# Optimization experiments

Measured on AMD Instinct MI355X. Metric: run time of the kernel, lower is better.

## Reference

```python
import jax, jax.numpy as jnp
import numpy as np

N_NODES = 100000
N_EDGES = 1600000
D = 128          # gnn_input_size == gnn_hidden_size
N_LAYERS = 7
N_GRAPHS = 64
N_CLASSES = 10
SNN_IN, SNN_H = 512, 1024
SNN_BETA = 0.85


def setup_inputs() -> dict:
    key = jax.random.key(0)
    ks = jax.random.split(key, 16)
    s = 0.05  # keep activations tame through 7 relu layers
    return {
        "snn_x": jax.random.normal(ks[0], (N_GRAPHS, SNN_IN), jnp.float32),
        "x": jax.random.normal(ks[1], (N_NODES, D), jnp.float32),
        "edge_index": jax.random.randint(ks[2], (2, N_EDGES), 0, N_NODES, jnp.int64),
        "batch": jnp.sort(jax.random.randint(ks[3], (N_NODES,), 0, N_GRAPHS, jnp.int64)),
        "snn_w1": jax.random.normal(ks[4], (SNN_IN, SNN_H), jnp.float32) * s,
        "snn_b1": jax.random.normal(ks[5], (SNN_H,), jnp.float32) * s,
        "snn_w2": jax.random.normal(ks[6], (SNN_H, N_CLASSES), jnp.float32) * s,
        "snn_b2": jax.random.normal(ks[7], (N_CLASSES,), jnp.float32) * s,
        "conv_wrel": jax.random.normal(ks[8], (N_LAYERS, D, D), jnp.float32) * s,
        "conv_wroot": jax.random.normal(ks[9], (N_LAYERS, D, D), jnp.float32) * s,
        "conv_brel": jax.random.normal(ks[10], (N_LAYERS, D), jnp.float32) * s,
        "lin_w": jax.random.normal(ks[11], (D, N_CLASSES), jnp.float32) * s,
        "lin_b": jax.random.normal(ks[12], (N_CLASSES,), jnp.float32) * s,
        "fuse_w": jax.random.normal(ks[13], (2 * N_CLASSES, N_CLASSES), jnp.float32) * s,
        "fuse_b": jax.random.normal(ks[14], (N_CLASSES,), jnp.float32) * s,
    }


def reference(snn_x, x, edge_index, batch,
              snn_w1, snn_b1, snn_w2, snn_b2,
              conv_wrel, conv_wroot, conv_brel,
              lin_w, lin_b, fuse_w, fuse_b):
    n = x.shape[0]
    src, dst = edge_index[0], edge_index[1]
    h = x
    for i in range(conv_wrel.shape[0]):
        agg = jax.ops.segment_sum(h[src], dst, num_segments=n)  # gather + scatter-add
        h = jax.nn.relu(agg @ conv_wrel[i] + conv_brel[i] + h @ conv_wroot[i])
    # global_mean_pool over batch segments
    sums = jax.ops.segment_sum(h, batch, num_segments=N_GRAPHS)
    cnts = jax.ops.segment_sum(jnp.ones((n,), h.dtype), batch, num_segments=N_GRAPHS)
    pooled = sums / jnp.maximum(cnts, 1.0)[:, None]
    gnn_logits = pooled @ lin_w + lin_b
    # SNN branch
    snn_h = jax.nn.relu(snn_x @ snn_w1 + snn_b1)
    snn_logits = SNN_BETA * (snn_h @ snn_w2 + snn_b2)
    # fusion
    fused = jnp.concatenate([snn_logits, gnn_logits], axis=-1)
    return fused @ fuse_w + fuse_b
```

## Files before the change

kernel.cpp:

```cpp
#include <hip/hip_runtime.h>
#include <hip/hip_bf16.h>

#define N_NODES 100000
#define N_EDGES 1600000
#define DIM     128
#define N_LAYERS 7
#define N_GRAPHS 64
#define SNN_IN  512
#define SNN_HID 1024
#define NCLS    10
#define M_PAD   100096
#define MBLK    782
#define NBK     782
#define SORT_CHUNK 4096
#define SORT_NCH   391
#define XPAIRS  (N_NODES * 64)
#define WELEMS  (N_LAYERS * DIM * 256)
#define AGG_BLOCKS 2048
#define AGG_WAVES  (AGG_BLOCKS * 4)
#define POOL_NB 782

typedef __attribute__((ext_vector_type(8))) short short8;
typedef __attribute__((ext_vector_type(4))) float f32x4;

__device__ __forceinline__ unsigned int f2bf(float f) {
    unsigned int u = __float_as_uint(f);
    return (u + 0x7fffu + ((u >> 16) & 1u)) >> 16;
}
__device__ __forceinline__ float bf2f(unsigned short b) {
    return __uint_as_float(((unsigned int)b) << 16);
}
__device__ __forceinline__ void acc_pair(unsigned int u, float& lo, float& hi) {
    lo += __uint_as_float(u << 16);
    hi += __uint_as_float(u & 0xffff0000u);
}

__global__ void k_convert(const float* __restrict__ x, const float* __restrict__ wrel,
                          const float* __restrict__ wroot, unsigned int* __restrict__ h,
                          unsigned short* __restrict__ Wt,
                          float* __restrict__ pooled, int* __restrict__ counts) {
    int i = blockIdx.x * blockDim.x + threadIdx.x;
    if (i < N_GRAPHS * 128) pooled[i] = 0.f;
    if (i >= N_GRAPHS * 128 && i < N_GRAPHS * 129) counts[i - N_GRAPHS * 128] = 0;
    if (i < XPAIRS) {
        float2 v = ((const float2*)x)[i];
        h[i] = f2bf(v.x) | (f2bf(v.y) << 16);
    } else {
        int idx = i - XPAIRS;
        if (idx < WELEMS) {
            int l = idx >> 15, rem = idx & 32767, n = rem >> 8, k = rem & 255;
            float v = (k < 128) ? wrel[l * 16384 + k * 128 + n]
                                : wroot[l * 16384 + (k - 128) * 128 + n];
            Wt[idx] = (unsigned short)f2bf(v);
        }
    }
}

__global__ __launch_bounds__(256) void k_histA(const int* __restrict__ dst,
                                               int* __restrict__ chunk_hist) {
    __shared__ int hist[NBK];
    int b = blockIdx.x, t = threadIdx.x;
    int e0 = b * SORT_CHUNK;
    int e1 = e0 + SORT_CHUNK; if (e1 > N_EDGES) e1 = N_EDGES;
    for (int i = t; i < NBK; i += 256) hist[i] = 0;
    __syncthreads();
    for (int e = e0 + t; e < e1; e += 256) atomicAdd(&hist[dst[e] >> 7], 1);
    __syncthreads();
    for (int i = t; i < NBK; i += 256) chunk_hist[b * NBK + i] = hist[i];
}

__global__ __launch_bounds__(64) void k_colscan(int* __restrict__ chunk_hist,
                                                int* __restrict__ btot) {
    int b = blockIdx.x;
    int lane = threadIdx.x;
    const int C = (SORT_NCH + 63) / 64;
    int vals[C]; int sum = 0;
    #pragma unroll
    for (int j = 0; j < C; j++) {
        int c = lane * C + j;
        vals[j] = (c < SORT_NCH) ? chunk_hist[c * NBK + b] : 0;
        sum += vals[j];
    }
    int s = sum;
    #pragma unroll
    for (int o = 1; o < 64; o <<= 1) { int t = __shfl_up(s, o); if (lane >= o) s += t; }
    if (lane == 63) btot[b] = s;
    int run = s - sum;
    #pragma unroll
    for (int j = 0; j < C; j++) {
        int c = lane * C + j;
        if (c < SORT_NCH) chunk_hist[c * NBK + b] = run;
        run += vals[j];
    }
}

__global__ __launch_bounds__(256) void k_bscan(const int* __restrict__ btot,
                                               int* __restrict__ bucket_base) {
    __shared__ int wsum[4];
    int tid = threadIdx.x, lane = tid & 63, wid = tid >> 6;
    int i0 = tid * 4;
    int v[4]; int sum = 0;
    #pragma unroll
    for (int j = 0; j < 4; j++) { int i = i0 + j; v[j] = (i < NBK) ? btot[i] : 0; sum += v[j]; }
    int s = sum;
    #pragma unroll
    for (int o = 1; o < 64; o <<= 1) { int t = __shfl_up(s, o); if (lane >= o) s += t; }
    if (lane == 63) wsum[wid] = s;
    __syncthreads();
    if (tid == 0) {
        int acc = 0;
        #pragma unroll
        for (int w = 0; w < 4; w++) { acc += wsum[w]; wsum[w] = acc; }
    }
    __syncthreads();
    int prefix = s - sum + (wid ? wsum[wid - 1] : 0);
    #pragma unroll
    for (int j = 0; j < 4; j++) { int i = i0 + j; if (i < NBK) bucket_base[i] = prefix; prefix += v[j]; }
}

__global__ __launch_bounds__(256) void k_scatterA(const int* __restrict__ src,
                                                  const int* __restrict__ dst,
                                                  const int* __restrict__ chunk_hist,
                                                  const int* __restrict__ bucket_base,
                                                  unsigned int* __restrict__ pairs) {
    __shared__ int lcur[NBK];
    int b = blockIdx.x, t = threadIdx.x;
    int e0 = b * SORT_CHUNK;
    int e1 = e0 + SORT_CHUNK; if (e1 > N_EDGES) e1 = N_EDGES;
    for (int i = t; i < NBK; i += 256) lcur[i] = chunk_hist[b * NBK + i] + bucket_base[i];
    __syncthreads();
    for (int e = e0 + t; e < e1; e += 256) {
        int d = dst[e];
        int bk = d >> 7;
        int pos = atomicAdd(&lcur[bk], 1);
        pairs[pos] = (unsigned int)src[e] | ((unsigned int)(d & 127) << 17);
    }
}

__global__ __launch_bounds__(256) void k_bucketB(const unsigned int* __restrict__ pairs,
                                                 const int* __restrict__ bucket_base,
                                                 const int* __restrict__ btot,
                                                 int* __restrict__ row_off,
                                                 int* __restrict__ sorted_src) {
    __shared__ int lcnt[128];
    __shared__ int loff[128];
    int b = blockIdx.x, t = threadIdx.x;
    int node0 = b << 7;
    int nn = N_NODES - node0; if (nn > 128) nn = 128;
    int base = bucket_base[b];
    int end  = base + btot[b];
    if (t < 128) lcnt[t] = 0;
    __syncthreads();
    for (int i = base + t; i < end; i += 256) atomicAdd(&lcnt[pairs[i] >> 17], 1);
    __syncthreads();
    if (t < 64) {
        int v0 = lcnt[2 * t], v1 = lcnt[2 * t + 1];
        int s = v0 + v1, ps = s;
        #pragma unroll
        for (int o = 1; o < 64; o <<= 1) { int u = __shfl_up(ps, o); if (t >= o) ps += u; }
        int excl = ps - s;
        loff[2 * t] = excl; loff[2 * t + 1] = excl + v0;
    }
    __syncthreads();
    if (t < nn) row_off[node0 + t] = base + loff[t];
    if (b == NBK - 1 && t == 0) row_off[N_NODES] = end;
    if (t < 128) lcnt[t] = 0;
    __syncthreads();
    for (int i = base + t; i < end; i += 256) {
        unsigned int p = pairs[i];
        int l = p >> 17;
        int pos = atomicAdd(&lcnt[l], 1);
        sorted_src[base + loff[l] + pos] = (int)(p & 0x1FFFFu);
    }
}

__global__ __launch_bounds__(256) void k_agg(const uint4* __restrict__ h4,
                                             const int* __restrict__ row_off,
                                             const int* __restrict__ sorted_src,
                                             uint4* __restrict__ agg4) {
    int gw = blockIdx.x * 4 + (threadIdx.x >> 6);
    int lane = threadIdx.x & 63;
    int sub = lane >> 4, li = lane & 15;
    for (int node = gw; node < N_NODES; node += AGG_WAVES) {
        int beg = row_off[node], end = row_off[node + 1];
        float a[8] = {0.f, 0.f, 0.f, 0.f, 0.f, 0.f, 0.f, 0.f};
        for (int base = beg; base < end; base += 16) {
            int sidx[4]; bool val[4];
            #pragma unroll
            for (int u = 0; u < 4; u++) {
                int e = base + 4 * u + sub;
                val[u] = e < end;
                sidx[u] = val[u] ? sorted_src[e] : 0;
            }
            uint4 r[4];
            #pragma unroll
            for (int u = 0; u < 4; u++) {
                if (val[u]) r[u] = h4[(size_t)sidx[u] * 16 + li];
                else        r[u] = make_uint4(0u, 0u, 0u, 0u);
            }
            #pragma unroll
            for (int u = 0; u < 4; u++) {
                acc_pair(r[u].x, a[0], a[1]); acc_pair(r[u].y, a[2], a[3]);
                acc_pair(r[u].z, a[4], a[5]); acc_pair(r[u].w, a[6], a[7]);
            }
        }
        #pragma unroll
        for (int i = 0; i < 8; i++) {
            a[i] += __shfl_xor(a[i], 16);
            a[i] += __shfl_xor(a[i], 32);
        }
        if (sub == 0) {
            uint4 o;
            o.x = f2bf(a[0]) | (f2bf(a[1]) << 16);
            o.y = f2bf(a[2]) | (f2bf(a[3]) << 16);
            o.z = f2bf(a[4]) | (f2bf(a[5]) << 16);
            o.w = f2bf(a[6]) | (f2bf(a[7]) << 16);
            agg4[(size_t)node * 16 + li] = o;
        }
    }
}

__global__ __launch_bounds__(256) void k_gemm(const unsigned short* __restrict__ Ag,
                                              const unsigned short* __restrict__ H,
                                              const unsigned short* __restrict__ Wt,
                                              const float* __restrict__ bias,
                                              unsigned short* __restrict__ Hout) {
    __shared__ unsigned short Es[64 * 144];
    int tid = threadIdx.x;
    int lane = tid & 63, wid = tid >> 6;
    int wr = (wid >> 1) * 64, wc = (wid & 1) * 64;
    int row0 = blockIdx.x * 128;
    f32x4 acc[4][4] = {};

    int ksub = (lane >> 4) * 8;
    const unsigned short* Aga = Ag + (size_t)(row0 + wr + (lane & 15)) * 128 + ksub;
    const unsigned short* Ha  = H  + (size_t)(row0 + wr + (lane & 15)) * 128 + ksub;
    const unsigned short* Bb  = Wt + (size_t)(wc + (lane & 15)) * 256 + ksub;

    auto load_frags = [&](short8* a, short8* b, int s) {
        const unsigned short* ab = (s < 4 ? Aga : Ha) + (s & 3) * 32;
        #pragma unroll
        for (int mi = 0; mi < 4; mi++) a[mi] = *(const short8*)(ab + mi * 16 * 128);
        const unsigned short* bp = Bb + s * 32;
        #pragma unroll
        for (int ni = 0; ni < 4; ni++) b[ni] = *(const short8*)(bp + ni * 16 * 256);
    };
    auto do_mfma = [&](short8* a, short8* b) {
        #pragma unroll
        for (int mi = 0; mi < 4; mi++)
            #pragma unroll
            for (int ni = 0; ni < 4; ni++)
                acc[mi][ni] = __builtin_amdgcn_mfma_f32_16x16x32_bf16(a[mi], b[ni], acc[mi][ni], 0, 0, 0);
    };

    short8 a0[4], b0[4], a1[4], b1[4];
    load_frags(a0, b0, 0);
    #pragma unroll
    for (int s = 0; s < 8; s += 2) {
        load_frags(a1, b1, s + 1);
        do_mfma(a0, b0);
        if (s + 2 < 8) load_frags(a0, b0, s + 2);
        do_mfma(a1, b1);
    }

    int cb = wc + (lane & 15);
    int rs = (lane >> 4) * 4;
    #pragma unroll
    for (int p = 0; p < 2; ++p) {
        __syncthreads();
        if (wr == 64 * p) {
            #pragma unroll
            for (int ni = 0; ni < 4; ni++) {
                int col = cb + ni * 16;
                float bn = bias[col];
                #pragma unroll
                for (int mi = 0; mi < 4; mi++) {
                    int rloc = mi * 16 + rs;
                    #pragma unroll
                    for (int rr = 0; rr < 4; rr++) {
                        float v = acc[mi][ni][rr] + bn;
                        v = v > 0.f ? v : 0.f;
                        Es[(rloc + rr) * 144 + col] = (unsigned short)f2bf(v);
                    }
                }
            }
        }
        __syncthreads();
        int rloc = tid >> 2;
        int c4 = (tid & 3) * 4;
        uint4* gd = (uint4*)(Hout + (size_t)(row0 + 64 * p + rloc) * 128);
        const uint4* es = (const uint4*)(Es + (size_t)rloc * 144);
        #pragma unroll
        for (int j = 0; j < 4; j++) gd[c4 + j] = es[c4 + j];
    }
}

__global__ __launch_bounds__(256) void k_pool_snn(const unsigned short* __restrict__ h,
                                                  const int* __restrict__ batch,
                                                  float* __restrict__ pooled,
                                                  int* __restrict__ counts,
                                                  const float* __restrict__ x,
                                                  const float* __restrict__ w1,
                                                  const float* __restrict__ b1,
                                                  float* __restrict__ snn_out) {
    if (blockIdx.x < POOL_NB) {
        __shared__ int bsh[128];
        int start = blockIdx.x * 128;
        int t = threadIdx.x & 127;
        int half = threadIdx.x >> 7;
        if (half == 0) {
            int end = start + 128; if (end > N_NODES) end = N_NODES;
            int nn = end - start;
            if (t < nn) bsh[t] = batch[start + t];
        }
        __syncthreads();
        if (half == 1) {
            int end = start + 128; if (end > N_NODES) end = N_NODES;
            int nn = end - start;
            float acc = 0.f; int cur = -1, cnt = 0;
            for (int i = 0; i < nn; i++) {
                int g = bsh[i];
                if (g != cur) {
                    if (cur >= 0) { atomicAdd(&pooled[cur * 128 + t], acc); if (t == 0) atomicAdd(&counts[cur], cnt); }
                    cur = g; acc = 0.f; cnt = 0;
                }
                acc += bf2f(h[(size_t)(start + i) * 128 + t]);
                cnt++;
            }
            if (cur >= 0) { atomicAdd(&pooled[cur * 128 + t], acc); if (t == 0) atomicAdd(&counts[cur], cnt); }
        } else {
            int end = start + 128; if (end > N_NODES) end = N_NODES;
            int nn = end - start;
            float acc = 0.f; int cur = -1;
            int td = t + 0;
            (void)nn; (void)acc; (void)cur; (void)td;
        }
    } else {
        int m = blockIdx.x - POOL_NB;
        __shared__ float xs[SNN_IN];
        int tid = threadIdx.x;
        for (int i = tid; i < SNN_IN; i += 256) xs[i] = x[m * SNN_IN + i];
        __syncthreads();
        float a0 = 0.f, a1 = 0.f, a2 = 0.f, a3 = 0.f;
        for (int k = 0; k < SNN_IN; k++) {
            float xv = xs[k];
            const float* wr = w1 + (size_t)k * SNN_HID + tid;
            a0 += xv * wr[0]; a1 += xv * wr[256]; a2 += xv * wr[512]; a3 += xv * wr[768];
        }
        float v;
        v = a0 + b1[tid];       snn_out[m * SNN_HID + tid]       = v > 0.f ? v : 0.f;
        v = a1 + b1[tid + 256]; snn_out[m * SNN_HID + tid + 256] = v > 0.f ? v : 0.f;
        v = a2 + b1[tid + 512]; snn_out[m * SNN_HID + tid + 512] = v > 0.f ? v : 0.f;
        v = a3 + b1[tid + 768]; snn_out[m * SNN_HID + tid + 768] = v > 0.f ? v : 0.f;
    }
}

__global__ __launch_bounds__(64) void k_head(const float* __restrict__ pooled, const int* __restrict__ counts,
                                             const float* __restrict__ lin_w, const float* __restrict__ lin_b,
                                             const float* __restrict__ snn_h, const float* __restrict__ w2,
                                             const float* __restrict__ b2, const float* __restrict__ fuse_w,
                                             const float* __restrict__ fuse_b, float* __restrict__ out) {
    int m = blockIdx.x, lane = threadIdx.x;
    __shared__ float sm[20];
    float cnt = (float)(counts[m] > 0 ? counts[m] : 1);
    float p0 = pooled[m * 128 + lane] / cnt;
    float p1 = pooled[m * 128 + 64 + lane] / cnt;
    for (int c = 0; c < NCLS; c++) {
        float v = p0 * lin_w[lane * 10 + c] + p1 * lin_w[(lane + 64) * 10 + c];
        #pragma unroll
        for (int o = 32; o > 0; o >>= 1) v += __shfl_down(v, o);
        if (lane == 0) sm[10 + c] = v + lin_b[c];
    }
    for (int c = 0; c < NCLS; c++) {
        float v = 0.f;
        #pragma unroll
        for (int j = 0; j < 16; j++) {
            int k = lane + j * 64;
            v += snn_h[m * SNN_HID + k] * w2[k * 10 + c];
        }
        #pragma unroll
        for (int o = 32; o > 0; o >>= 1) v += __shfl_down(v, o);
        if (lane == 0) sm[c] = 0.85f * (v + b2[c]);
    }
    __syncthreads();
    if (lane < NCLS) {
        float o = fuse_b[lane];
        #pragma unroll
        for (int j = 0; j < 20; j++) o += sm[j] * fuse_w[j * 10 + lane];
        out[m * 10 + lane] = o;
    }
}

extern "C" void kernel_launch(void* const* d_in, const int* in_sizes, int n_in,
                              void* d_out, int out_size, void* d_ws, size_t ws_size,
                              hipStream_t stream) {
    const float* snn_x  = (const float*)d_in[0];
    const float* x      = (const float*)d_in[1];
    const int*   ei     = (const int*)d_in[2];
    const int*   batch  = (const int*)d_in[3];
    const float* w1     = (const float*)d_in[4];
    const float* b1     = (const float*)d_in[5];
    const float* w2     = (const float*)d_in[6];
    const float* b2     = (const float*)d_in[7];
    const float* wrel   = (const float*)d_in[8];
    const float* wroot  = (const float*)d_in[9];
    const float* brel   = (const float*)d_in[10];
    const float* lin_w  = (const float*)d_in[11];
    const float* lin_b  = (const float*)d_in[12];
    const float* fuse_w = (const float*)d_in[13];
    const float* fuse_b = (const float*)d_in[14];
    const int* srcv = ei;
    const int* dstv = ei + N_EDGES;

    char* ws = (char*)d_ws;
    size_t off = 0;
    auto alloc = [&](size_t b) { char* p = ws + off; off = (off + b + 255) & ~(size_t)255; return p; };
    unsigned short* h0   = (unsigned short*)alloc((size_t)M_PAD * 128 * 2);
    unsigned short* h1   = (unsigned short*)alloc((size_t)M_PAD * 128 * 2);
    unsigned short* agg  = (unsigned short*)alloc((size_t)M_PAD * 128 * 2);
    unsigned short* Wt   = (unsigned short*)alloc((size_t)N_LAYERS * 128 * 256 * 2);
    int* sorted_src = (int*)alloc((size_t)N_EDGES * 4);
    unsigned int* pairs = (unsigned int*)alloc((size_t)N_EDGES * 4);
    int* chunk_hist = (int*)alloc((size_t)SORT_NCH * NBK * 4);
    int* row_off    = (int*)alloc((size_t)(N_NODES + 1) * 4);
    int* btot       = (int*)alloc((size_t)NBK * 4);
    int* bucket_base= (int*)alloc((size_t)NBK * 4);
    float* pooled   = (float*)alloc((size_t)N_GRAPHS * 128 * 4);
    int* counts     = (int*)alloc((size_t)N_GRAPHS * 4);
    float* snn_h    = (float*)alloc((size_t)N_GRAPHS * SNN_HID * 4);

    k_histA<<<SORT_NCH, 256, 0, stream>>>(dstv, chunk_hist);
    k_colscan<<<NBK, 64, 0, stream>>>(chunk_hist, btot);
    k_bscan<<<1, 256, 0, stream>>>(btot, bucket_base);
    k_scatterA<<<SORT_NCH, 256, 0, stream>>>(srcv, dstv, chunk_hist, bucket_base, pairs);
    k_bucketB<<<NBK, 256, 0, stream>>>(pairs, bucket_base, btot, row_off, sorted_src);
    k_convert<<<(XPAIRS + WELEMS + 255) / 256, 256, 0, stream>>>(x, wrel, wroot, (unsigned int*)h0,
                                                                 Wt, pooled, counts);

    unsigned short* hc = h0;
    unsigned short* hn = h1;
    for (int l = 0; l < N_LAYERS; l++) {
        k_agg<<<AGG_BLOCKS, 256, 0, stream>>>((const uint4*)hc, row_off, sorted_src, (uint4*)agg);
        k_gemm<<<MBLK, 256, 0, stream>>>(agg, hc, Wt + (size_t)l * 128 * 256, brel + l * 128, hn);
        unsigned short* t = hc; hc = hn; hn = t;
    }
    k_pool_snn<<<POOL_NB + N_GRAPHS, 256, 0, stream>>>(hc, batch, pooled, counts,
                                                       snn_x, w1, b1, snn_h);
    k_head<<<N_GRAPHS, 64, 0, stream>>>(pooled, counts, lin_w, lin_b, snn_h, w2, b2, fuse_w, fuse_b,
                                        (float*)d_out);
}
```

Before: 924.8 us.

## Pad CSR rows to multiples of four and aggregate four nodes per wave

```diff
diff --git a/kernel.cpp b/kernel.cpp
--- a/kernel.cpp
+++ b/kernel.cpp
@@ -15,10 +15,13 @@
 #define SORT_CHUNK 4096
 #define SORT_NCH   391
 #define XPAIRS  (N_NODES * 64)
+#define HPAIRS  (M_PAD * 64)
 #define WELEMS  (N_LAYERS * DIM * 256)
 #define AGG_BLOCKS 2048
 #define AGG_WAVES  (AGG_BLOCKS * 4)
+#define NQUAD   (N_NODES / 4)
 #define POOL_NB 782
+#define SS_PAD  2000384
 
 typedef __attribute__((ext_vector_type(8))) short short8;
 typedef __attribute__((ext_vector_type(4))) float f32x4;
@@ -45,8 +48,10 @@
     if (i < XPAIRS) {
         float2 v = ((const float2*)x)[i];
         h[i] = f2bf(v.x) | (f2bf(v.y) << 16);
+    } else if (i < HPAIRS) {
+        h[i] = 0u;
     } else {
-        int idx = i - XPAIRS;
+        int idx = i - HPAIRS;
         if (idx < WELEMS) {
             int l = idx >> 15, rem = idx & 32767, n = rem >> 8, k = rem & 255;
             float v = (k < 128) ? wrel[l * 16384 + k * 128 + n]
@@ -141,6 +146,7 @@
                                                  const int* __restrict__ bucket_base,
                                                  const int* __restrict__ btot,
                                                  int* __restrict__ row_off,
+                                                 int* __restrict__ ndeg,
                                                  int* __restrict__ sorted_src) {
     __shared__ int lcnt[128];
     __shared__ int loff[128];
@@ -149,12 +155,13 @@
     int nn = N_NODES - node0; if (nn > 128) nn = 128;
     int base = bucket_base[b];
     int end  = base + btot[b];
+    int pbase = ((base + 3) & ~3) + 512 * b;
     if (t < 128) lcnt[t] = 0;
     __syncthreads();
     for (int i = base + t; i < end; i += 256) atomicAdd(&lcnt[pairs[i] >> 17], 1);
     __syncthreads();
     if (t < 64) {
-        int v0 = lcnt[2 * t], v1 = lcnt[2 * t + 1];
+        int v0 = (lcnt[2 * t] + 3) & ~3, v1 = (lcnt[2 * t + 1] + 3) & ~3;
         int s = v0 + v1, ps = s;
         #pragma unroll
         for (int o = 1; o < 64; o <<= 1) { int u = __shfl_up(ps, o); if (t >= o) ps += u; }
@@ -162,61 +169,81 @@
         loff[2 * t] = excl; loff[2 * t + 1] = excl + v0;
     }
     __syncthreads();
-    if (t < nn) row_off[node0 + t] = base + loff[t];
-    if (b == NBK - 1 && t == 0) row_off[N_NODES] = end;
+    if (t < nn) {
+        int d = lcnt[t];
+        row_off[node0 + t] = pbase + loff[t];
+        ndeg[node0 + t] = d;
+        int pad = (d + 3) & ~3;
+        for (int k = d; k < pad; k++) sorted_src[pbase + loff[t] + k] = N_NODES;
+    }
+    __syncthreads();
     if (t < 128) lcnt[t] = 0;
     __syncthreads();
     for (int i = base + t; i < end; i += 256) {
         unsigned int p = pairs[i];
         int l = p >> 17;
         int pos = atomicAdd(&lcnt[l], 1);
-        sorted_src[base + loff[l] + pos] = (int)(p & 0x1FFFFu);
-    }
-}
-
-__global__ __launch_bounds__(256) void k_agg(const uint4* __restrict__ h4,
+        sorted_src[pbase + loff[l] + pos] = (int)(p & 0x1FFFFu);
+    }
+}
+
+#define GATH(d0, d1, d2, d3, s) \
+    d0 = *(const uint4*)(hbl + (size_t)(((unsigned)(s).x) << 8)); \
+    d1 = *(const uint4*)(hbl + (size_t)(((unsigned)(s).y) << 8)); \
+    d2 = *(const uint4*)(hbl + (size_t)(((unsigned)(s).z) << 8)); \
+    d3 = *(const uint4*)(hbl + (size_t)(((unsigned)(s).w) << 8));
+#define ACC4(r0, r1, r2, r3) \
+    acc_pair((r0).x, a[0], a[1]); acc_pair((r0).y, a[2], a[3]); \
+    acc_pair((r0).z, a[4], a[5]); acc_pair((r0).w, a[6], a[7]); \
+    acc_pair((r1).x, a[0], a[1]); acc_pair((r1).y, a[2], a[3]); \
+    acc_pair((r1).z, a[4], a[5]); acc_pair((r1).w, a[6], a[7]); \
+    acc_pair((r2).x, a[0], a[1]); acc_pair((r2).y, a[2], a[3]); \
+    acc_pair((r2).z, a[4], a[5]); acc_pair((r2).w, a[6], a[7]); \
+    acc_pair((r3).x, a[0], a[1]); acc_pair((r3).y, a[2], a[3]); \
+    acc_pair((r3).z, a[4], a[5]); acc_pair((r3).w, a[6], a[7]);
+
+__global__ __launch_bounds__(256) void k_agg(const char* __restrict__ hb,
                                              const int* __restrict__ row_off,
-                                             const int* __restrict__ sorted_src,
+                                             const int* __restrict__ ndeg,
+                                             const int4* __restrict__ sorted4,
                                              uint4* __restrict__ agg4) {
     int gw = blockIdx.x * 4 + (threadIdx.x >> 6);
     int lane = threadIdx.x & 63;
     int sub = lane >> 4, li = lane & 15;
-    for (int node = gw; node < N_NODES; node += AGG_WAVES) {
-        int beg = row_off[node], end = row_off[node + 1];
+    const char* hbl = hb + li * 16;
+    for (int quad = gw; quad < NQUAD; quad += AGG_WAVES) {
+        int node = quad * 4 + sub;
+        int beg = row_off[node] >> 2;
+        int nit = (ndeg[node] + 3) >> 2;
         float a[8] = {0.f, 0.f, 0.f, 0.f, 0.f, 0.f, 0.f, 0.f};
-        for (int base = beg; base < end; base += 16) {
-            int sidx[4]; bool val[4];
-            #pragma unroll
-            for (int u = 0; u < 4; u++) {
-                int e = base + 4 * u + sub;
-                val[u] = e < end;
-                sidx[u] = val[u] ? sorted_src[e] : 0;
+        if (nit > 0) {
+            int4 sa = sorted4[beg];
+            int4 sb = sorted4[beg + 1];
+            uint4 A0, A1, A2, A3, B0, B1, B2, B3;
+            GATH(A0, A1, A2, A3, sa);
+            int it = 0;
+            for (; it + 2 < nit; it += 2) {
+                GATH(B0, B1, B2, B3, sb);
+                sa = sorted4[beg + it + 2];
+                ACC4(A0, A1, A2, A3);
+                GATH(A0, A1, A2, A3, sa);
+                sb = sorted4[beg + it + 3];
+                ACC4(B0, B1, B2, B3);
             }
-            uint4 r[4];
-            #pragma unroll
-            for (int u = 0; u < 4; u++) {
-                if (val[u]) r[u] = h4[(size_t)sidx[u] * 16 + li];
-                else        r[u] = make_uint4(0u, 0u, 0u, 0u);
+            if (it + 1 < nit) {
+                GATH(B0, B1, B2, B3, sb);
+                ACC4(A0, A1, A2, A3);
+                ACC4(B0, B1, B2, B3);
+            } else {
+                ACC4(A0, A1, A2, A3);
             }
-            #pragma unroll
-            for (int u = 0; u < 4; u++) {
-                acc_pair(r[u].x, a[0], a[1]); acc_pair(r[u].y, a[2], a[3]);
-                acc_pair(r[u].z, a[4], a[5]); acc_pair(r[u].w, a[6], a[7]);
-            }
-        }
-        #pragma unroll
-        for (int i = 0; i < 8; i++) {
-            a[i] += __shfl_xor(a[i], 16);
-            a[i] += __shfl_xor(a[i], 32);
-        }
-        if (sub == 0) {
-            uint4 o;
-            o.x = f2bf(a[0]) | (f2bf(a[1]) << 16);
-            o.y = f2bf(a[2]) | (f2bf(a[3]) << 16);
-            o.z = f2bf(a[4]) | (f2bf(a[5]) << 16);
-            o.w = f2bf(a[6]) | (f2bf(a[7]) << 16);
-            agg4[(size_t)node * 16 + li] = o;
-        }
+        }
+        uint4 o;
+        o.x = f2bf(a[0]) | (f2bf(a[1]) << 16);
+        o.y = f2bf(a[2]) | (f2bf(a[3]) << 16);
+        o.z = f2bf(a[4]) | (f2bf(a[5]) << 16);
+        o.w = f2bf(a[6]) | (f2bf(a[7]) << 16);
+        agg4[(size_t)node * 16 + li] = o;
     }
 }
 
@@ -280,6 +307,7 @@
                     for (int rr = 0; rr < 4; rr++) {
                         float v = acc[mi][ni][rr] + bn;
                         v = v > 0.f ? v : 0.f;
+                        if (row0 + 64 * p + rloc + rr >= N_NODES) v = 0.f;
                         Es[(rloc + rr) * 144 + col] = (unsigned short)f2bf(v);
                     }
                 }
@@ -328,12 +356,6 @@
                 cnt++;
             }
             if (cur >= 0) { atomicAdd(&pooled[cur * 128 + t], acc); if (t == 0) atomicAdd(&counts[cur], cnt); }
-        } else {
-            int end = start + 128; if (end > N_NODES) end = N_NODES;
-            int nn = end - start;
-            float acc = 0.f; int cur = -1;
-            int td = t + 0;
-            (void)nn; (void)acc; (void)cur; (void)td;
         }
     } else {
         int m = blockIdx.x - POOL_NB;
@@ -419,10 +441,11 @@
     unsigned short* h1   = (unsigned short*)alloc((size_t)M_PAD * 128 * 2);
     unsigned short* agg  = (unsigned short*)alloc((size_t)M_PAD * 128 * 2);
     unsigned short* Wt   = (unsigned short*)alloc((size_t)N_LAYERS * 128 * 256 * 2);
-    int* sorted_src = (int*)alloc((size_t)N_EDGES * 4);
+    int* sorted_src = (int*)alloc((size_t)SS_PAD * 4 + 16);
     unsigned int* pairs = (unsigned int*)alloc((size_t)N_EDGES * 4);
     int* chunk_hist = (int*)alloc((size_t)SORT_NCH * NBK * 4);
     int* row_off    = (int*)alloc((size_t)(N_NODES + 1) * 4);
+    int* ndeg       = (int*)alloc((size_t)N_NODES * 4);
     int* btot       = (int*)alloc((size_t)NBK * 4);
     int* bucket_base= (int*)alloc((size_t)NBK * 4);
     float* pooled   = (float*)alloc((size_t)N_GRAPHS * 128 * 4);
@@ -433,14 +456,15 @@
     k_colscan<<<NBK, 64, 0, stream>>>(chunk_hist, btot);
     k_bscan<<<1, 256, 0, stream>>>(btot, bucket_base);
     k_scatterA<<<SORT_NCH, 256, 0, stream>>>(srcv, dstv, chunk_hist, bucket_base, pairs);
-    k_bucketB<<<NBK, 256, 0, stream>>>(pairs, bucket_base, btot, row_off, sorted_src);
-    k_convert<<<(XPAIRS + WELEMS + 255) / 256, 256, 0, stream>>>(x, wrel, wroot, (unsigned int*)h0,
+    k_bucketB<<<NBK, 256, 0, stream>>>(pairs, bucket_base, btot, row_off, ndeg, sorted_src);
+    k_convert<<<(HPAIRS + WELEMS + 255) / 256, 256, 0, stream>>>(x, wrel, wroot, (unsigned int*)h0,
                                                                  Wt, pooled, counts);
 
     unsigned short* hc = h0;
     unsigned short* hn = h1;
     for (int l = 0; l < N_LAYERS; l++) {
-        k_agg<<<AGG_BLOCKS, 256, 0, stream>>>((const uint4*)hc, row_off, sorted_src, (uint4*)agg);
+        k_agg<<<AGG_BLOCKS, 256, 0, stream>>>((const char*)hc, row_off, ndeg,
+                                              (const int4*)sorted_src, (uint4*)agg);
         k_gemm<<<MBLK, 256, 0, stream>>>(agg, hc, Wt + (size_t)l * 128 * 256, brel + l * 128, hn);
         unsigned short* t = hc; hc = hn; hn = t;
     }
```

Result: no change. 932.5 us (+0.8%).
